# Kernel tuning notes

Hardware: AMD Instinct MI355X
Metric: run time of the kernel (lower is better)

## Reference

```python
import jax, jax.numpy as jnp
import numpy as np

SCALING = 32.0 / 16.0  # alpha / rank

def setup_inputs() -> dict:
    key = jax.random.key(0)
    k1, k2, k3, k4 = jax.random.split(key, 4)
    B_, S, D_in, D_out, R = 4, 4096, 2048, 2048, 16
    x = jax.random.normal(k1, (B_, S, D_in), dtype=jnp.float32)
    # dequantized 4-bit base weight, torch Linear layout [out, in]
    W_base = jax.random.normal(k2, (D_out, D_in), dtype=jnp.float32) * 0.02
    A = jax.random.normal(k3, (R, D_in), dtype=jnp.float32) * (1.0 / np.sqrt(D_in))
    # torch code zero-inits lora_B, but use random for nontrivial gradient checking
    B = jax.random.normal(k4, (D_out, R), dtype=jnp.float32) * 0.02
    return {"x": x, "W_base": W_base, "A": A, "B": B}

def reference(x, W_base, A, B):
    # base: Y = x @ W_base^T   [b, s, out]
    base = jnp.einsum('bsd,od->bso', x, W_base)
    # LoRA: (x @ A^T) @ B^T * scaling   (rank is tiny, keep factored)
    lora = jnp.einsum('bsr,or->bso', jnp.einsum('bsd,rd->bsr', x, A), B)
    return base + lora * SCALING
```

## Files before the change

kernel.cpp:

```cpp
#include <hip/hip_runtime.h>


typedef __bf16 bf16x8 __attribute__((ext_vector_type(8)));
typedef float  f32x4  __attribute__((ext_vector_type(4)));
typedef unsigned short u16x8 __attribute__((ext_vector_type(8)));

#define AS1C(p) ((const __attribute__((address_space(1))) void*)(p))
#define AS3(p)  ((__attribute__((address_space(3))) void*)(p))

__device__ __forceinline__ unsigned short f2bf_rne(float f) {
  unsigned int u = __float_as_uint(f);
  u += 0x7FFFu + ((u >> 16) & 1u);
  return (unsigned short)(u >> 16);
}

constexpr int M_ = 16384;
constexpr int N_ = 2048;
constexpr int K_ = 2048;
constexpr int R_ = 16;
constexpr float SCALING = 2.0f;

constexpr int BM = 128, BN = 128, BK = 64;

__global__ __launch_bounds__(256) void cvt_kernel(const float* __restrict__ in,
                                                  unsigned short* __restrict__ out) {
  size_t i = (size_t)blockIdx.x * blockDim.x + threadIdx.x;
  const float4* p = (const float4*)in;
  float4 a = p[2 * i];
  float4 b = p[2 * i + 1];
  u16x8 o;
  o[0] = f2bf_rne(a.x); o[1] = f2bf_rne(a.y); o[2] = f2bf_rne(a.z); o[3] = f2bf_rne(a.w);
  o[4] = f2bf_rne(b.x); o[5] = f2bf_rne(b.y); o[6] = f2bf_rne(b.z); o[7] = f2bf_rne(b.w);
  ((u16x8*)out)[i] = o;
}

__global__ __launch_bounds__(256) void weff_kernel(const float* __restrict__ W,
                                                   const float* __restrict__ A,
                                                   const float* __restrict__ Bl,
                                                   unsigned short* __restrict__ out) {
  int idx = blockIdx.x * blockDim.x + threadIdx.x;
  int o = idx >> 11;
  int d = idx & 2047;
  float acc = W[idx];
#pragma unroll
  for (int r = 0; r < R_; ++r)
    acc = fmaf(SCALING * Bl[o * R_ + r], A[r * K_ + d], acc);
  out[idx] = f2bf_rne(acc);
}

__global__ __launch_bounds__(256) void gemm_kernel(const unsigned short* __restrict__ X,
                                                   const unsigned short* __restrict__ W,
                                                   float* __restrict__ C) {
  __shared__ __align__(16) unsigned short As[BM * BK];
  __shared__ __align__(16) unsigned short Bs[BN * BK];

  const int tid  = threadIdx.x;
  const int wave = tid >> 6;
  const int lane = tid & 63;

  const int id   = blockIdx.x + gridDim.x * blockIdx.y;
  const int xcd  = id & 7;
  const int slot = id >> 3;
  const int bm   = (xcd * 16 + (slot >> 4)) * BM;
  const int bn   = (slot & 15) * BN;

  const int wm = (wave & 1) * 64;
  const int wn = (wave >> 1) * 64;

  f32x4 acc[4][4] = {};

  const int r8 = lane >> 3;
  const int gseg = ((lane & 7) - r8) & 7;

  const unsigned short* xst = X + (size_t)(bm + wave * 32 + r8) * K_ + gseg * 8;
  const unsigned short* wst = W + (size_t)(bn + wave * 32 + r8) * K_ + gseg * 8;
  unsigned short* lA = &As[(wave * 32) * BK];
  unsigned short* lB = &Bs[(wave * 32) * BK];

  const int fm   = lane & 15;
  const int quad = lane >> 4;

  for (int k0 = 0; k0 < K_; k0 += BK) {
#pragma unroll
    for (int c = 0; c < 4; ++c)
      __builtin_amdgcn_global_load_lds(AS1C(xst + (size_t)(c * 8) * K_ + k0),
                                       AS3(lA + c * 8 * BK), 16, 0, 0);
#pragma unroll
    for (int c = 0; c < 4; ++c)
      __builtin_amdgcn_global_load_lds(AS1C(wst + (size_t)(c * 8) * K_ + k0),
                                       AS3(lB + c * 8 * BK), 16, 0, 0);
    __syncthreads();

#pragma unroll
    for (int t = 0; t < 2; ++t) {
      const int sp = ((4 * t + quad + fm) & 7) * 8;
      bf16x8 af[4], bfr[4];
#pragma unroll
      for (int i = 0; i < 4; ++i)
        af[i] = *(const bf16x8*)&As[(wm + i * 16 + fm) * BK + sp];
#pragma unroll
      for (int j = 0; j < 4; ++j)
        bfr[j] = *(const bf16x8*)&Bs[(wn + j * 16 + fm) * BK + sp];

#pragma unroll
      for (int i = 0; i < 4; ++i)
#pragma unroll
        for (int j = 0; j < 4; ++j)
          acc[i][j] = __builtin_amdgcn_mfma_f32_16x16x32_bf16(af[i], bfr[j], acc[i][j], 0, 0, 0);
    }

    __syncthreads();
  }

  const int r0   = quad * 4;
  const int col0 = fm;
#pragma unroll
  for (int i = 0; i < 4; ++i) {
#pragma unroll
    for (int j = 0; j < 4; ++j) {
      size_t base = (size_t)(bm + wm + i * 16 + r0) * N_ + (size_t)(bn + wn + j * 16 + col0);
#pragma unroll
      for (int r = 0; r < 4; ++r)
        __builtin_nontemporal_store(acc[i][j][r], &C[base + (size_t)r * N_]);
    }
  }
}

extern "C" void kernel_launch(void* const* d_in, const int* in_sizes, int n_in,
                              void* d_out, int out_size, void* d_ws, size_t ws_size,
                              hipStream_t stream) {
  const float* x  = (const float*)d_in[0];
  const float* W  = (const float*)d_in[1];
  const float* A  = (const float*)d_in[2];
  const float* Bl = (const float*)d_in[3];
  float* out = (float*)d_out;

  unsigned short* Xb   = (unsigned short*)d_ws;
  unsigned short* Weff = Xb + (size_t)M_ * K_;

  cvt_kernel<<<(int)((size_t)M_ * K_ / 8 / 256), 256, 0, stream>>>(x, Xb);
  weff_kernel<<<(N_ * K_) / 256, 256, 0, stream>>>(W, A, Bl, Weff);

  dim3 grid(N_ / BN, M_ / BM);
  gemm_kernel<<<grid, 256, 0, stream>>>(Xb, Weff, out);
}
```

Measured before the change: 384.9 us.

## Use 256x256 tiles with 8 waves and double-buffered pipelined LDS staging

Replaces the 128x128 single-buffered GEMM with a 256x256 tile computed by 512 threads. Shared memory is double-buffered, and each of the eight phases per K-tile pair issues global-to-LDS loads for a later tile while running MFMAs on the current quarter tile. Phases are coordinated with explicit vmcnt/lgkmcnt waits, barriers and setprio. The aim is to hide memory latency and raise data reuse per loaded byte. The cost is 128KB of LDS per block, a larger accumulator footprint that raises register pressure, and fragile hand-placed wait counts.

```diff
diff --git a/kernel.cpp b/kernel.cpp
--- a/kernel.cpp
+++ b/kernel.cpp
@@ -20,7 +20,8 @@
 constexpr int R_ = 16;
 constexpr float SCALING = 2.0f;
 
-constexpr int BM = 128, BN = 128, BK = 64;
+constexpr int BM = 256, BN = 256, BK = 64;
+constexpr int NT = K_ / BK;
 
 __global__ __launch_bounds__(256) void cvt_kernel(const float* __restrict__ in,
                                                   unsigned short* __restrict__ out) {
@@ -48,82 +49,126 @@
   out[idx] = f2bf_rne(acc);
 }
 
-__global__ __launch_bounds__(256) void gemm_kernel(const unsigned short* __restrict__ X,
-                                                   const unsigned short* __restrict__ W,
-                                                   float* __restrict__ C) {
-  __shared__ __align__(16) unsigned short As[BM * BK];
-  __shared__ __align__(16) unsigned short Bs[BN * BK];
+__global__ __launch_bounds__(512, 2) void gemm_kernel(const unsigned short* __restrict__ X,
+                                                      const unsigned short* __restrict__ W,
+                                                      float* __restrict__ C) {
+  __shared__ __align__(16) unsigned short sA[2][BM * BK];
+  __shared__ __align__(16) unsigned short sB[2][BN * BK];
 
   const int tid  = threadIdx.x;
-  const int wave = tid >> 6;
+  const int w    = tid >> 6;
   const int lane = tid & 63;
-
-  const int id   = blockIdx.x + gridDim.x * blockIdx.y;
-  const int xcd  = id & 7;
-  const int slot = id >> 3;
-  const int bm   = (xcd * 16 + (slot >> 4)) * BM;
-  const int bn   = (slot & 15) * BN;
-
-  const int wm = (wave & 1) * 64;
-  const int wn = (wave >> 1) * 64;
-
-  f32x4 acc[4][4] = {};
-
-  const int r8 = lane >> 3;
-  const int gseg = ((lane & 7) - r8) & 7;
-
-  const unsigned short* xst = X + (size_t)(bm + wave * 32 + r8) * K_ + gseg * 8;
-  const unsigned short* wst = W + (size_t)(bn + wave * 32 + r8) * K_ + gseg * 8;
-  unsigned short* lA = &As[(wave * 32) * BK];
-  unsigned short* lB = &Bs[(wave * 32) * BK];
-
   const int fm   = lane & 15;
   const int quad = lane >> 4;
 
-  for (int k0 = 0; k0 < K_; k0 += BK) {
-#pragma unroll
-    for (int c = 0; c < 4; ++c)
-      __builtin_amdgcn_global_load_lds(AS1C(xst + (size_t)(c * 8) * K_ + k0),
-                                       AS3(lA + c * 8 * BK), 16, 0, 0);
-#pragma unroll
-    for (int c = 0; c < 4; ++c)
-      __builtin_amdgcn_global_load_lds(AS1C(wst + (size_t)(c * 8) * K_ + k0),
-                                       AS3(lB + c * 8 * BK), 16, 0, 0);
-    __syncthreads();
+  const int id = blockIdx.x;
+  const int bm = ((id & 7) * 8 + (id >> 6)) * BM;
+  const int bn = ((id >> 3) & 7) * BN;
 
-#pragma unroll
-    for (int t = 0; t < 2; ++t) {
-      const int sp = ((4 * t + quad + fm) & 7) * 8;
-      bf16x8 af[4], bfr[4];
-#pragma unroll
-      for (int i = 0; i < 4; ++i)
-        af[i] = *(const bf16x8*)&As[(wm + i * 16 + fm) * BK + sp];
-#pragma unroll
-      for (int j = 0; j < 4; ++j)
-        bfr[j] = *(const bf16x8*)&Bs[(wn + j * 16 + fm) * BK + sp];
+  const int wrow = (w >> 2) * 128;
+  const int wcol = (w & 3) * 64;
 
-#pragma unroll
-      for (int i = 0; i < 4; ++i)
-#pragma unroll
-        for (int j = 0; j < 4; ++j)
-          acc[i][j] = __builtin_amdgcn_mfma_f32_16x16x32_bf16(af[i], bfr[j], acc[i][j], 0, 0, 0);
-    }
+  const int strow = tid >> 3;
+  const int gseg  = ((tid & 7) - strow) & 7;
+  const int brow0 = 64 * (tid >> 8) + (strow & 31);
 
-    __syncthreads();
+  const unsigned short* xa = X + (size_t)(bm + strow) * K_ + gseg * 8;
+  const unsigned short* xb = W + (size_t)(bn + brow0) * K_ + gseg * 8;
+
+  const int aw = w * 8 * BK;
+  const int bw = ((w >> 2) * 64 + (w & 3) * 8) * BK;
+
+  const int sp0 = ((quad + fm) & 7) * 8;
+  const int sp1 = ((quad + fm + 4) & 7) * 8;
+
+  f32x4 acc[8][4] = {};
+
+#define STAGE_A(hm, kt, b) do {                                                   \
+    __builtin_amdgcn_global_load_lds(AS1C(xa + (size_t)((hm) * 64) * K_ + (kt) * BK), \
+        AS3(&sA[b][((hm) * 64) * BK + aw]), 16, 0, 0);                            \
+    __builtin_amdgcn_global_load_lds(AS1C(xa + (size_t)((hm) * 64 + 128) * K_ + (kt) * BK), \
+        AS3(&sA[b][((hm) * 64 + 128) * BK + aw]), 16, 0, 0);                      \
+  } while (0)
+
+#define STAGE_B(hn, kt, b) do {                                                   \
+    __builtin_amdgcn_global_load_lds(AS1C(xb + (size_t)((hn) * 32) * K_ + (kt) * BK), \
+        AS3(&sB[b][((hn) * 32) * BK + bw]), 16, 0, 0);                            \
+    __builtin_amdgcn_global_load_lds(AS1C(xb + (size_t)((hn) * 32 + 128) * K_ + (kt) * BK), \
+        AS3(&sB[b][((hn) * 32 + 128) * BK + bw]), 16, 0, 0);                      \
+  } while (0)
+
+#define PHASE(tb, hm, hn, STAGE) do {                                             \
+    bf16x8 af[4][2], bv[2][2];                                                    \
+    _Pragma("unroll")                                                             \
+    for (int i2 = 0; i2 < 4; ++i2) {                                              \
+      const int ra = (wrow + (hm) * 64 + i2 * 16 + fm) * BK;                      \
+      af[i2][0] = *(const bf16x8*)&sA[tb][ra + sp0];                              \
+      af[i2][1] = *(const bf16x8*)&sA[tb][ra + sp1];                              \
+    }                                                                             \
+    _Pragma("unroll")                                                             \
+    for (int j2 = 0; j2 < 2; ++j2) {                                              \
+      const int rb = (wcol + (hn) * 32 + j2 * 16 + fm) * BK;                      \
+      bv[j2][0] = *(const bf16x8*)&sB[tb][rb + sp0];                              \
+      bv[j2][1] = *(const bf16x8*)&sB[tb][rb + sp1];                              \
+    }                                                                             \
+    STAGE;                                                                        \
+    __builtin_amdgcn_s_barrier();                                                 \
+    asm volatile("s_waitcnt lgkmcnt(0)" ::: "memory");                            \
+    __builtin_amdgcn_s_setprio(1);                                                \
+    _Pragma("unroll")                                                             \
+    for (int i2 = 0; i2 < 4; ++i2)                                                \
+      _Pragma("unroll")                                                           \
+      for (int j2 = 0; j2 < 2; ++j2) {                                            \
+        acc[(hm) * 4 + i2][(hn) * 2 + j2] = __builtin_amdgcn_mfma_f32_16x16x32_bf16( \
+            af[i2][0], bv[j2][0], acc[(hm) * 4 + i2][(hn) * 2 + j2], 0, 0, 0);    \
+        acc[(hm) * 4 + i2][(hn) * 2 + j2] = __builtin_amdgcn_mfma_f32_16x16x32_bf16( \
+            af[i2][1], bv[j2][1], acc[(hm) * 4 + i2][(hn) * 2 + j2], 0, 0, 0);    \
+      }                                                                           \
+    __builtin_amdgcn_s_setprio(0);                                                \
+    asm volatile("s_waitcnt vmcnt(8)" ::: "memory");                              \
+    __builtin_amdgcn_s_barrier();                                                 \
+  } while (0)
+
+  STAGE_B(0, 0, 0);
+  STAGE_A(0, 0, 0);
+  STAGE_A(1, 0, 0);
+  STAGE_B(1, 0, 0);
+  STAGE_B(0, 1, 1);
+  STAGE_A(0, 1, 1);
+  asm volatile("s_waitcnt vmcnt(8)" ::: "memory");
+  __builtin_amdgcn_s_barrier();
+
+#pragma unroll 1
+  for (int it = 0; it < NT / 2; ++it) {
+    const int t1 = 2 * it + 1;
+    const int t2 = (2 * it + 2 < NT) ? 2 * it + 2 : NT - 1;
+    const int t3 = (2 * it + 3 < NT) ? 2 * it + 3 : NT - 1;
+    PHASE(0, 0, 0, STAGE_A(1, t1, 1));
+    PHASE(0, 1, 0, STAGE_B(1, t1, 1));
+    PHASE(0, 0, 1, STAGE_B(0, t2, 0));
+    PHASE(0, 1, 1, STAGE_A(0, t2, 0));
+    PHASE(1, 0, 0, STAGE_A(1, t2, 0));
+    PHASE(1, 1, 0, STAGE_B(1, t2, 0));
+    PHASE(1, 0, 1, STAGE_B(0, t3, 1));
+    PHASE(1, 1, 1, STAGE_A(0, t3, 1));
   }
 
-  const int r0   = quad * 4;
-  const int col0 = fm;
+  asm volatile("s_waitcnt vmcnt(0)" ::: "memory");
+
+  const int r0 = quad * 4;
 #pragma unroll
-  for (int i = 0; i < 4; ++i) {
+  for (int i = 0; i < 8; ++i) {
 #pragma unroll
     for (int j = 0; j < 4; ++j) {
-      size_t base = (size_t)(bm + wm + i * 16 + r0) * N_ + (size_t)(bn + wn + j * 16 + col0);
+      size_t base = (size_t)(bm + wrow + i * 16 + r0) * N_ + (size_t)(bn + wcol + j * 16 + fm);
 #pragma unroll
       for (int r = 0; r < 4; ++r)
         __builtin_nontemporal_store(acc[i][j][r], &C[base + (size_t)r * N_]);
     }
   }
+#undef PHASE
+#undef STAGE_A
+#undef STAGE_B
 }
 
 extern "C" void kernel_launch(void* const* d_in, const int* in_sizes, int n_in,
@@ -141,6 +186,5 @@
   cvt_kernel<<<(int)((size_t)M_ * K_ / 8 / 256), 256, 0, stream>>>(x, Xb);
   weff_kernel<<<(N_ * K_) / 256, 256, 0, stream>>>(W, A, Bl, Weff);
 
-  dim3 grid(N_ / BN, M_ / BM);
-  gemm_kernel<<<grid, 256, 0, stream>>>(Xb, Weff, out);
+  gemm_kernel<<<(M_ / BM) * (N_ / BN), 512, 0, stream>>>(Xb, Weff, out);
 }
```

Measured after the change: 405.2 us. 5.3% more time.
